# Kernel optimization log

Hardware: AMD Instinct MI355X
Metric: run time of the kernel (lower is better)

## Reference

```python
import jax, jax.numpy as jnp
import numpy as np

EMBED_DIM = 1024
NUM_HEADS = 16
HEAD_DIM = EMBED_DIM // NUM_HEADS


def setup_inputs() -> dict:
    key = jax.random.key(0)
    ks = jax.random.split(key, 11)
    B, T, C = 2, 2048, EMBED_DIM
    s = 1.0 / np.sqrt(C)  # ~ torch Linear init scale
    inp = {
        "q": jax.random.normal(ks[0], (B, T, C), jnp.float32),
        "k": jax.random.normal(ks[1], (B, T, C), jnp.float32),
        "v": jax.random.normal(ks[2], (B, T, C), jnp.float32),
        "Wq": jax.random.normal(ks[3], (C, C), jnp.float32) * s,
        "bq": jax.random.normal(ks[4], (C,), jnp.float32) * s,
        "Wk": jax.random.normal(ks[5], (C, C), jnp.float32) * s,
        "bk": jax.random.normal(ks[6], (C,), jnp.float32) * s,
        "Wv": jax.random.normal(ks[7], (C, C), jnp.float32) * s,
        "bv": jax.random.normal(ks[8], (C,), jnp.float32) * s,
        "Wo": jax.random.normal(ks[9], (C, C), jnp.float32) * s,
        "bo": jax.random.normal(ks[10], (C,), jnp.float32) * s,
    }
    return inp


def _split_heads(x):
    B, T, C = x.shape
    return x.reshape(B, T, NUM_HEADS, HEAD_DIM).transpose(0, 2, 1, 3)  # [B,H,T,Dh]


def reference(q, k, v, Wq, bq, Wk, bk, Wv, bv, Wo, bo):
    B, Tq, C = q.shape
    # torch Linear: y = x @ W.T + b
    qh = _split_heads(q @ Wq.T + bq)
    kh = _split_heads(k @ Wk.T + bk)
    vh = _split_heads(v @ Wv.T + bv)
    scale = 1.0 / np.sqrt(HEAD_DIM).astype(np.float32)
    logits = jnp.einsum("bhqd,bhkd->bhqk", qh, kh) * scale
    attn = jax.nn.softmax(logits, axis=-1)
    out = jnp.einsum("bhqk,bhkd->bhqd", attn, vh)
    out = out.transpose(0, 2, 1, 3).reshape(B, Tq, C)
    return out @ Wo.T + bo
```

## Files before the change

kernel.cpp:

```cpp
#include <hip/hip_runtime.h>
#include <stdint.h>

#define T_SEQ 2048
#define CDIM 1024
#define NHEAD 16
#define HDIM 64
#define MROWS 4096

typedef unsigned short u16;
typedef __attribute__((ext_vector_type(8))) short bf16x8;
typedef __attribute__((ext_vector_type(4))) float f32x4;
typedef __attribute__((ext_vector_type(16))) float f32x16;
typedef __attribute__((ext_vector_type(4))) unsigned short u16x4;
typedef __attribute__((ext_vector_type(4))) unsigned int uint4v;

#if __has_builtin(__builtin_amdgcn_exp2f)
#define EXP2(x) __builtin_amdgcn_exp2f(x)
#else
#define EXP2(x) exp2f(x)
#endif

__device__ __forceinline__ u16 f2bf(float f) {
  unsigned u = __builtin_bit_cast(unsigned, f);
  u += 0x7fffu + ((u >> 16) & 1u);
  return (u16)(u >> 16);
}

__device__ __forceinline__ float bf2f(unsigned hw) {
  return __builtin_bit_cast(float, hw << 16);
}

__device__ __forceinline__ unsigned cvt_pk_bf16(float lo, float hi) {
  unsigned r;
  asm("v_cvt_pk_bf16_f32 %0, %1, %2" : "=v"(r) : "v"(lo), "v"(hi));
  return r;
}

__device__ __forceinline__ void pls(unsigned &a, unsigned &b) {
  asm("v_permlane32_swap_b32 %0, %1" : "+v"(a), "+v"(b));
}

__device__ __forceinline__ void gll16(const void* g, void* l) {
  __builtin_amdgcn_global_load_lds((__attribute__((address_space(1))) void*)(g),
                                   (__attribute__((address_space(3))) void*)(l),
                                   16, 0, 0);
}

__device__ __forceinline__ void wg_barrier() {
  asm volatile("" ::: "memory");
  __builtin_amdgcn_s_barrier();
  asm volatile("" ::: "memory");
}

#define WAIT_VM(N) do { __builtin_amdgcn_s_waitcnt(0xF00 | 0x70 | (N)); \
                        asm volatile("" ::: "memory"); } while (0)

__global__ __launch_bounds__(256)
void cvt_all(const float* __restrict__ q, const float* __restrict__ k, const float* __restrict__ v,
             const float* __restrict__ wq, const float* __restrict__ wk,
             const float* __restrict__ wv, const float* __restrict__ wo,
             u16* __restrict__ qb, u16* __restrict__ kb, u16* __restrict__ vb,
             u16* __restrict__ wqb, u16* __restrict__ wkb, u16* __restrict__ wvb, u16* __restrict__ wob) {
  int b = blockIdx.x;
  const float* src; u16* dst; int base;
  if (b < 1536) {
    int s = b >> 9;
    src = (s == 0) ? q : (s == 1) ? k : v;
    dst = (s == 0) ? qb : (s == 1) ? kb : vb;
    base = (b & 511) * 2048;
  } else {
    int s = (b - 1536) >> 7;
    src = (s == 0) ? wq : (s == 1) ? wk : (s == 2) ? wv : wo;
    dst = (s == 0) ? wqb : (s == 1) ? wkb : (s == 2) ? wvb : wob;
    base = ((b - 1536) & 127) * 2048;
  }
#pragma unroll
  for (int j = 0; j < 8; ++j) {
    int i = base + j * 256 + threadIdx.x;
    float4 a = ((const float4*)src)[i];
    u16x4 o = { f2bf(a.x), f2bf(a.y), f2bf(a.z), f2bf(a.w) };
    ((u16x4*)dst)[i] = o;
  }
}


__device__ __forceinline__ void gemm_stage(const u16* Ag, const u16* Bg, u16* Ad, u16* Bd) {
#pragma unroll
  for (int c = 0; c < 4; ++c) {
    gll16(Ag + c * 32 * CDIM, Ad + c * 2048);
    gll16(Bg + c * 32 * CDIM, Bd + c * 2048);
  }
}

__device__ __forceinline__ void gemm_compute(const u16* As, const u16* Bs,
                                             f32x4 (&acc)[4][4],
                                             int wr, int wc, int lg, int lr) {
#pragma unroll
  for (int kk = 0; kk < 2; ++kk) {
    bf16x8 af[4], bfr[4];
#pragma unroll
    for (int f = 0; f < 4; ++f) {
      int ra = wr * 64 + f * 16 + lr;
      af[f]  = *(const bf16x8*)((const char*)As + ra * 128 + ((lg * 16 + kk * 64) ^ ((ra & 7) << 4)));
      int rb = wc * 64 + f * 16 + lr;
      bfr[f] = *(const bf16x8*)((const char*)Bs + rb * 128 + ((lg * 16 + kk * 64) ^ ((rb & 7) << 4)));
    }
#pragma unroll
    for (int i = 0; i < 4; ++i)
#pragma unroll
      for (int j = 0; j < 4; ++j)
        acc[i][j] = __builtin_amdgcn_mfma_f32_16x16x32_bf16(af[i], bfr[j], acc[i][j], 0, 0, 0);
  }
}

#define GEMM_KLOOP(As, Bs, Ad0, Bd0, Ad1, Bd1)                                 \
  gemm_stage(Ag, Bg, Ad0, Bd0);                                                \
  _Pragma("unroll 1")                                                          \
  for (int kt = 0; kt < 16; ++kt) {                                            \
    wg_barrier();                                                              \
    int nt = (kt + 1 < 16) ? kt + 1 : 15;                                      \
    if (kt & 1) gemm_stage(Ag + nt * 64, Bg + nt * 64, Ad0, Bd0);              \
    else        gemm_stage(Ag + nt * 64, Bg + nt * 64, Ad1, Bd1);              \
    WAIT_VM(8);                                                                \
    wg_barrier();                                                              \
    gemm_compute((kt & 1) ? As[1] : As[0], (kt & 1) ? Bs[1] : Bs[0],           \
                 acc, wr, wc, lg, lr);                                         \
  }

__global__ __launch_bounds__(256)
void gemm_qkv(const u16* __restrict__ A0, const u16* __restrict__ A1, const u16* __restrict__ A2,
              const u16* __restrict__ W0, const u16* __restrict__ W1, const u16* __restrict__ W2,
              const float* __restrict__ b0, const float* __restrict__ b1, const float* __restrict__ b2,
              u16* __restrict__ o0, u16* __restrict__ o1, u16* __restrict__ o2,
              float qscale) {
  __shared__ u16 As[2][128 * 64];
  __shared__ u16 Bs[2][128 * 64];
  const int z = blockIdx.z;
  const u16* A   = (z == 0) ? A0 : (z == 1) ? A1 : A2;
  const u16* Bw  = (z == 0) ? W0 : (z == 1) ? W1 : W2;
  const float* bias = (z == 0) ? b0 : (z == 1) ? b1 : b2;
  u16* outp = (z == 0) ? o0 : (z == 1) ? o1 : o2;
  const float scale = (z == 0) ? qscale : 1.0f;

  const int m0 = blockIdx.y * 128;
  const int n0 = blockIdx.x * 128;
  const int tid = threadIdx.x;
  const int w = tid >> 6, l = tid & 63;
  const int wr = w >> 1, wc = w & 1;
  const int lg = l >> 4, lr = l & 15;

  const int row0 = tid >> 3, slot0 = tid & 7;
  const int so = (slot0 ^ (row0 & 7)) << 3;
  const u16* Ag = A  + ((size_t)(m0 + row0)) * CDIM + so;
  const u16* Bg = Bw + ((size_t)(n0 + row0)) * CDIM + so;
  u16* Ad0 = As[0] + w * 512;  u16* Bd0 = Bs[0] + w * 512;
  u16* Ad1 = As[1] + w * 512;  u16* Bd1 = Bs[1] + w * 512;

  f32x4 acc[4][4] = {};

  GEMM_KLOOP(As, Bs, Ad0, Bd0, Ad1, Bd1)

#pragma unroll
  for (int fj = 0; fj < 4; ++fj) {
    int col = n0 + wc * 64 + fj * 16 + lr;
    float bv = bias[col];
    int h = col >> 6, d = col & 63;
#pragma unroll
    for (int fi = 0; fi < 4; ++fi) {
#pragma unroll
      for (int i = 0; i < 4; ++i) {
        int row = m0 + wr * 64 + fi * 16 + lg * 4 + i;
        float val = (acc[fi][fj][i] + bv) * scale;
        int b = row >> 11, t = row & 2047;
        if (z < 2)
          outp[(((size_t)(b * NHEAD + h)) * T_SEQ + t) * HDIM + d] = f2bf(val);
        else
          outp[(((size_t)(b * NHEAD + h)) * HDIM + d) * T_SEQ + t] = f2bf(val);
      }
    }
  }
}

__global__ __launch_bounds__(256)
void gemm_bt0(const u16* __restrict__ A, const u16* __restrict__ Bw,
              const float* __restrict__ bias, float* __restrict__ outp) {
  __shared__ u16 As[2][128 * 64];
  __shared__ u16 Bs[2][128 * 64];
  const int m0 = blockIdx.y * 128;
  const int n0 = blockIdx.x * 128;
  const int tid = threadIdx.x;
  const int w = tid >> 6, l = tid & 63;
  const int wr = w >> 1, wc = w & 1;
  const int lg = l >> 4, lr = l & 15;

  const int row0 = tid >> 3, slot0 = tid & 7;
  const int so = (slot0 ^ (row0 & 7)) << 3;
  const u16* Ag = A  + ((size_t)(m0 + row0)) * CDIM + so;
  const u16* Bg = Bw + ((size_t)(n0 + row0)) * CDIM + so;
  u16* Ad0 = As[0] + w * 512;  u16* Bd0 = Bs[0] + w * 512;
  u16* Ad1 = As[1] + w * 512;  u16* Bd1 = Bs[1] + w * 512;

  f32x4 acc[4][4] = {};

  GEMM_KLOOP(As, Bs, Ad0, Bd0, Ad1, Bd1)

#pragma unroll
  for (int fj = 0; fj < 4; ++fj) {
    int col = n0 + wc * 64 + fj * 16 + lr;
    float bv = bias[col];
#pragma unroll
    for (int fi = 0; fi < 4; ++fi) {
#pragma unroll
      for (int i = 0; i < 4; ++i) {
        int row = m0 + wr * 64 + fi * 16 + lg * 4 + i;
        outp[(size_t)row * CDIM + col] = acc[fi][fj][i] + bv;
      }
    }
  }
}


__device__ __forceinline__ void attn_tile(const char* Kb, const char* Vb,
                                          const bf16x8 (&qf)[4],
                                          f32x16 (&acc)[2], f32x4& lsum, float& m_run,
                                          int lo5, int hi, int swz) {
  f32x16 s[2] = {};
  const int colK = 16 * hi;
  __builtin_amdgcn_s_setprio(1);
#pragma unroll
  for (int st = 0; st < 4; ++st) {
    bf16x8 k0 = *(const bf16x8*)(Kb + lo5 * 128        + ((32 * st + colK) ^ swz));
    bf16x8 k1 = *(const bf16x8*)(Kb + (lo5 + 32) * 128 + ((32 * st + colK) ^ swz));
    s[0] = __builtin_amdgcn_mfma_f32_32x32x16_bf16(k0, qf[st], s[0], 0, 0, 0);
    s[1] = __builtin_amdgcn_mfma_f32_32x32x16_bf16(k1, qf[st], s[1], 0, 0, 0);
  }
  __builtin_amdgcn_s_setprio(0);

  float t[8];
#pragma unroll
  for (int i = 0; i < 8; ++i)
    t[i] = fmaxf(fmaxf(s[0][2 * i], s[0][2 * i + 1]), fmaxf(s[1][2 * i], s[1][2 * i + 1]));
  float u0 = fmaxf(fmaxf(t[0], t[1]), fmaxf(t[2], t[3]));
  float u1 = fmaxf(fmaxf(t[4], t[5]), fmaxf(t[6], t[7]));
  float tl = fmaxf(u0, u1);
  if (!__all(tl <= m_run + 8.f)) {
    float tmax = fmaxf(tl, __shfl_xor(tl, 32));
    float m_new = fmaxf(m_run, tmax);
    float alpha = EXP2(m_run - m_new);
    lsum[0] *= alpha; lsum[1] *= alpha; lsum[2] *= alpha; lsum[3] *= alpha;
#pragma unroll
    for (int i = 0; i < 16; ++i) { acc[0][i] *= alpha; acc[1][i] *= alpha; }
    m_run = m_new;
  }

  unsigned pg[2][8];
#pragma unroll
  for (int g = 0; g < 8; ++g) {
    float a0 = EXP2(s[0][2 * g] - m_run), b0 = EXP2(s[0][2 * g + 1] - m_run);
    float a1 = EXP2(s[1][2 * g] - m_run), b1 = EXP2(s[1][2 * g + 1] - m_run);
    lsum[g & 3] += (a0 + b0) + (a1 + b1);
    pg[0][g] = cvt_pk_bf16(a0, b0);
    pg[1][g] = cvt_pk_bf16(a1, b1);
  }

  bf16x8 pb[4];
#pragma unroll
  for (int sub = 0; sub < 2; ++sub)
#pragma unroll
    for (int ks = 0; ks < 2; ++ks) {
      unsigned w0 = pg[sub][4 * ks + 0], w1 = pg[sub][4 * ks + 1];
      unsigned w2 = pg[sub][4 * ks + 2], w3 = pg[sub][4 * ks + 3];
      pls(w0, w2); pls(w1, w3);
      uint4v tt = { w0, w1, w2, w3 };
      pb[2 * sub + ks] = __builtin_bit_cast(bf16x8, tt);
    }

  __builtin_amdgcn_s_setprio(1);
#pragma unroll
  for (int ks = 0; ks < 4; ++ks) {
    bf16x8 v0 = *(const bf16x8*)(Vb + lo5 * 128        + ((32 * ks + colK) ^ swz));
    bf16x8 v1 = *(const bf16x8*)(Vb + (lo5 + 32) * 128 + ((32 * ks + colK) ^ swz));
    acc[0] = __builtin_amdgcn_mfma_f32_32x32x16_bf16(v0, pb[ks], acc[0], 0, 0, 0);
    acc[1] = __builtin_amdgcn_mfma_f32_32x32x16_bf16(v1, pb[ks], acc[1], 0, 0, 0);
  }
  __builtin_amdgcn_s_setprio(0);
}

__global__ __launch_bounds__(256, 4)
void attn_fused(const u16* __restrict__ Qh, const u16* __restrict__ Kh,
                const u16* __restrict__ Vt, u16* __restrict__ Op,
                float2* __restrict__ ml) {
  __shared__ u16 Ks[2][64 * 64];
  __shared__ u16 Vs[2][64 * 64];
  const int bh = blockIdx.y;
  const int q0 = blockIdx.x * 128;
  const int half = blockIdx.z;
  const int tid = threadIdx.x;
  const int w = tid >> 6, l = tid & 63;
  const int lo5 = l & 31, hi = l >> 5;
  const int swz = (l & 7) << 4;

  const u16* qptr = Qh + ((size_t)bh * T_SEQ + q0 + w * 32 + lo5) * HDIM + hi * 8;
  bf16x8 qf[4];
#pragma unroll
  for (int s = 0; s < 4; ++s) qf[s] = *(const bf16x8*)(qptr + 16 * s);

  const int srow = (w & 1) * 32 + (l >> 3);
  const int soff = ((l & 7) ^ ((l >> 3) & 7)) << 3;
  const u16* Kgs = Kh + ((size_t)bh * T_SEQ + srow) * HDIM + soff;
  const u16* Vgs = Vt + ((size_t)bh * HDIM + srow) * T_SEQ + soff;
  const int isV = w >> 1;

  auto stage = [&](int t, int db) {
    if (!isV) {
      u16* dst = Ks[db] + (w & 1) * 32 * 64;
      const u16* src = Kgs + (size_t)t * 64 * HDIM;
#pragma unroll
      for (int j = 0; j < 4; ++j)
        gll16(src + j * 8 * HDIM, dst + j * 8 * 64);
    } else {
      u16* dst = Vs[db] + (w & 1) * 32 * 64;
      const u16* src = Vgs + t * 64;
#pragma unroll
      for (int j = 0; j < 4; ++j)
        gll16(src + (size_t)j * 8 * T_SEQ, dst + j * 8 * 64);
    }
  };

  f32x16 acc[2] = {};
  f32x4 lsum = {};
  float m_run = -1e30f;
  const int tb = half * 16;

  stage(tb, 0);
#pragma unroll 1
  for (int s = 0; s < 16; ++s) {
    wg_barrier();
    int ns = (s + 1 < 16) ? s + 1 : 15;
    stage(tb + ns, (s + 1) & 1);
    WAIT_VM(4);
    wg_barrier();
    attn_tile((const char*)Ks[s & 1], (const char*)Vs[s & 1],
              qf, acc, lsum, m_run, lo5, hi, swz);
  }

  float ls = (lsum[0] + lsum[1]) + (lsum[2] + lsum[3]);
  ls += __shfl_xor(ls, 32);
  float inv = 1.f / ls;

  wg_barrier();
  char* os = (char*)&Ks[0][0] + w * 4096;
#pragma unroll
  for (int dsub = 0; dsub < 2; ++dsub)
#pragma unroll
    for (int gg = 0; gg < 4; ++gg) {
      unsigned wa = cvt_pk_bf16(acc[dsub][4 * gg + 0] * inv, acc[dsub][4 * gg + 1] * inv);
      unsigned wb = cvt_pk_bf16(acc[dsub][4 * gg + 2] * inv, acc[dsub][4 * gg + 3] * inv);
      uint2 wv = { wa, wb };
      int byte = lo5 * 128 + (((32 * dsub + 8 * gg + 4 * hi) * 2) ^ swz);
      *(uint2*)(os + byte) = wv;
    }
  u16* orow = Op + ((size_t)(half * 32 + bh) * T_SEQ + q0 + w * 32) * HDIM;
#pragma unroll
  for (int c = 0; c < 4; ++c) {
    int qq = 8 * c + (l >> 3);
    uint4v ov = *(const uint4v*)(os + qq * 128 + ((16 * (l & 7)) ^ ((qq & 7) << 4)));
    *(uint4v*)(orow + qq * HDIM + (l & 7) * 8) = ov;
  }
  if (hi == 0)
    ml[(size_t)(half * 32 + bh) * T_SEQ + q0 + w * 32 + lo5] = make_float2(m_run, ls);
}

__global__ __launch_bounds__(256)
void attn_combine(const u16* __restrict__ Op, const float2* __restrict__ ml,
                  u16* __restrict__ Ao) {
  int task0 = blockIdx.x * 256 + threadIdx.x;
#pragma unroll 1
  for (int it = 0; it < 4; ++it) {
    int task = task0 + it * 131072;
    int chunk = task & 7;
    int q  = (task >> 3) & 2047;
    int bh = task >> 14;
    float2 ml0 = ml[(size_t)bh * T_SEQ + q];
    float2 ml1 = ml[(size_t)(32 + bh) * T_SEQ + q];
    float M = fmaxf(ml0.x, ml1.x);
    float w0 = EXP2(ml0.x - M) * ml0.y;
    float w1 = EXP2(ml1.x - M) * ml1.y;
    float zi = 1.f / (w0 + w1);
    float a0 = w0 * zi, a1 = w1 * zi;
    const u16* p0 = Op + ((size_t)bh * T_SEQ + q) * HDIM + chunk * 8;
    const u16* p1 = Op + ((size_t)(32 + bh) * T_SEQ + q) * HDIM + chunk * 8;
    uint4v o0 = *(const uint4v*)p0;
    uint4v o1 = *(const uint4v*)p1;
    uint4v ov;
#pragma unroll
    for (int j = 0; j < 4; ++j) {
      float lo = a0 * bf2f(o0[j] & 0xffffu)  + a1 * bf2f(o1[j] & 0xffffu);
      float hi = a0 * bf2f(o0[j] >> 16)      + a1 * bf2f(o1[j] >> 16);
      ov[j] = cvt_pk_bf16(lo, hi);
    }
    int b = bh >> 4, h = bh & 15;
    *(uint4v*)(Ao + ((size_t)(b * T_SEQ + q)) * CDIM + h * HDIM + chunk * 8) = ov;
  }
}

extern "C" void kernel_launch(void* const* d_in, const int* in_sizes, int n_in,
                              void* d_out, int out_size, void* d_ws, size_t ws_size,
                              hipStream_t stream) {
  const float* q  = (const float*)d_in[0];
  const float* k  = (const float*)d_in[1];
  const float* v  = (const float*)d_in[2];
  const float* Wq = (const float*)d_in[3];
  const float* bq = (const float*)d_in[4];
  const float* Wk = (const float*)d_in[5];
  const float* bk = (const float*)d_in[6];
  const float* Wv = (const float*)d_in[7];
  const float* bv = (const float*)d_in[8];
  const float* Wo = (const float*)d_in[9];
  const float* bo = (const float*)d_in[10];

  char* ws = (char*)d_ws;
  size_t off = 0;
  auto alloc = [&](size_t n) { void* p = ws + off; off += (n + 255) & ~(size_t)255; return p; };
  const size_t NX = (size_t)MROWS * CDIM;
  const size_t NW = (size_t)CDIM * CDIM;
  u16* qb  = (u16*)alloc(NX * 2);
  u16* kb  = (u16*)alloc(NX * 2);
  u16* vb  = (u16*)alloc(NX * 2);
  u16* Wqb = (u16*)alloc(NW * 2);
  u16* Wkb = (u16*)alloc(NW * 2);
  u16* Wvb = (u16*)alloc(NW * 2);
  u16* Wob = (u16*)alloc(NW * 2);
  u16* Qhp = (u16*)alloc(NX * 2);
  u16* Khp = (u16*)alloc(NX * 2);
  u16* Vtp = (u16*)alloc(NX * 2);
  u16* Aop = (u16*)alloc(NX * 2);

  u16* Op = qb;
  float2* mlp = (float2*)vb;

  cvt_all<<<2048, 256, 0, stream>>>(q, k, v, Wq, Wk, Wv, Wo,
                                    qb, kb, vb, Wqb, Wkb, Wvb, Wob);

  const float qscale = 0.18033688011112042f;
  gemm_qkv<<<dim3(CDIM / 128, MROWS / 128, 3), 256, 0, stream>>>(
      qb, kb, vb, Wqb, Wkb, Wvb, bq, bk, bv, Qhp, Khp, Vtp, qscale);

  attn_fused<<<dim3(T_SEQ / 128, 32, 2), 256, 0, stream>>>(Qhp, Khp, Vtp, Op, mlp);
  attn_combine<<<512, 256, 0, stream>>>(Op, mlp, Aop);

  gemm_bt0<<<dim3(CDIM / 128, MROWS / 128), 256, 0, stream>>>(Aop, Wob, bo, (float*)d_out);

  (void)in_sizes; (void)n_in; (void)out_size; (void)ws_size;
}
```

Baseline: 132.8 us.

## Stage GEMM tiles through registers with single LDS buffer instead of direct-to-LDS loads

```diff
diff --git a/kernel.cpp b/kernel.cpp
--- a/kernel.cpp
+++ b/kernel.cpp
@@ -53,6 +53,8 @@
 }
 
 #define WAIT_VM(N) do { __builtin_amdgcn_s_waitcnt(0xF00 | 0x70 | (N)); \
+                        asm volatile("" ::: "memory"); } while (0)
+#define WAIT_LGKM0 do { __builtin_amdgcn_s_waitcnt(0xC07F); \
                         asm volatile("" ::: "memory"); } while (0)
 
 __global__ __launch_bounds__(256)
@@ -84,11 +86,22 @@
 }
 
 
-__device__ __forceinline__ void gemm_stage(const u16* Ag, const u16* Bg, u16* Ad, u16* Bd) {
+__device__ __forceinline__ void gemm_loads(const u16* Ag, const u16* Bg,
+                                           uint4v (&ar)[4], uint4v (&br)[4]) {
 #pragma unroll
   for (int c = 0; c < 4; ++c) {
-    gll16(Ag + c * 32 * CDIM, Ad + c * 2048);
-    gll16(Bg + c * 32 * CDIM, Bd + c * 2048);
+    ar[c] = *(const uint4v*)(Ag + c * 32 * CDIM);
+    br[c] = *(const uint4v*)(Bg + c * 32 * CDIM);
+  }
+}
+
+__device__ __forceinline__ void gemm_writes(u16* Ad, u16* Bd,
+                                            const uint4v (&ar)[4], const uint4v (&br)[4],
+                                            int tid) {
+#pragma unroll
+  for (int c = 0; c < 4; ++c) {
+    *(uint4v*)(Ad + (size_t)(c * 256 + tid) * 8) = ar[c];
+    *(uint4v*)(Bd + (size_t)(c * 256 + tid) * 8) = br[c];
   }
 }
 
@@ -113,18 +126,25 @@
   }
 }
 
-#define GEMM_KLOOP(As, Bs, Ad0, Bd0, Ad1, Bd1)                                 \
-  gemm_stage(Ag, Bg, Ad0, Bd0);                                                \
+#define GEMM_KLOOP_RS(Asb, Bsb)                                                \
+  uint4v ar[4], br[4];                                                         \
+  gemm_loads(Ag, Bg, ar, br);                                                  \
+  WAIT_VM(0);                                                                  \
+  gemm_writes(Asb, Bsb, ar, br, tid);                                          \
+  WAIT_LGKM0;                                                                  \
+  wg_barrier();                                                                \
   _Pragma("unroll 1")                                                          \
   for (int kt = 0; kt < 16; ++kt) {                                            \
+    int nt = (kt + 1 < 16) ? kt + 1 : 15;                                      \
+    gemm_loads(Ag + nt * 64, Bg + nt * 64, ar, br);                            \
+    gemm_compute(Asb, Bsb, acc, wr, wc, lg, lr);                               \
+    WAIT_VM(0);                                                                \
     wg_barrier();                                                              \
-    int nt = (kt + 1 < 16) ? kt + 1 : 15;                                      \
-    if (kt & 1) gemm_stage(Ag + nt * 64, Bg + nt * 64, Ad0, Bd0);              \
-    else        gemm_stage(Ag + nt * 64, Bg + nt * 64, Ad1, Bd1);              \
-    WAIT_VM(8);                                                                \
-    wg_barrier();                                                              \
-    gemm_compute((kt & 1) ? As[1] : As[0], (kt & 1) ? Bs[1] : Bs[0],           \
-                 acc, wr, wc, lg, lr);                                         \
+    if (kt < 15) {                                                             \
+      gemm_writes(Asb, Bsb, ar, br, tid);                                      \
+      WAIT_LGKM0;                                                              \
+      wg_barrier();                                                            \
+    }                                                                          \
   }
 
 __global__ __launch_bounds__(256)
@@ -133,8 +153,8 @@
               const float* __restrict__ b0, const float* __restrict__ b1, const float* __restrict__ b2,
               u16* __restrict__ o0, u16* __restrict__ o1, u16* __restrict__ o2,
               float qscale) {
-  __shared__ u16 As[2][128 * 64];
-  __shared__ u16 Bs[2][128 * 64];
+  __shared__ u16 Asb[128 * 64];
+  __shared__ u16 Bsb[128 * 64];
   const int z = blockIdx.z;
   const u16* A   = (z == 0) ? A0 : (z == 1) ? A1 : A2;
   const u16* Bw  = (z == 0) ? W0 : (z == 1) ? W1 : W2;
@@ -153,12 +173,10 @@
   const int so = (slot0 ^ (row0 & 7)) << 3;
   const u16* Ag = A  + ((size_t)(m0 + row0)) * CDIM + so;
   const u16* Bg = Bw + ((size_t)(n0 + row0)) * CDIM + so;
-  u16* Ad0 = As[0] + w * 512;  u16* Bd0 = Bs[0] + w * 512;
-  u16* Ad1 = As[1] + w * 512;  u16* Bd1 = Bs[1] + w * 512;
 
   f32x4 acc[4][4] = {};
 
-  GEMM_KLOOP(As, Bs, Ad0, Bd0, Ad1, Bd1)
+  GEMM_KLOOP_RS(Asb, Bsb)
 
 #pragma unroll
   for (int fj = 0; fj < 4; ++fj) {
@@ -184,8 +202,8 @@
 __global__ __launch_bounds__(256)
 void gemm_bt0(const u16* __restrict__ A, const u16* __restrict__ Bw,
               const float* __restrict__ bias, float* __restrict__ outp) {
-  __shared__ u16 As[2][128 * 64];
-  __shared__ u16 Bs[2][128 * 64];
+  __shared__ u16 Asb[128 * 64];
+  __shared__ u16 Bsb[128 * 64];
   const int m0 = blockIdx.y * 128;
   const int n0 = blockIdx.x * 128;
   const int tid = threadIdx.x;
@@ -197,12 +215,10 @@
   const int so = (slot0 ^ (row0 & 7)) << 3;
   const u16* Ag = A  + ((size_t)(m0 + row0)) * CDIM + so;
   const u16* Bg = Bw + ((size_t)(n0 + row0)) * CDIM + so;
-  u16* Ad0 = As[0] + w * 512;  u16* Bd0 = Bs[0] + w * 512;
-  u16* Ad1 = As[1] + w * 512;  u16* Bd1 = Bs[1] + w * 512;
 
   f32x4 acc[4][4] = {};
 
-  GEMM_KLOOP(As, Bs, Ad0, Bd0, Ad1, Bd1)
+  GEMM_KLOOP_RS(Asb, Bsb)
 
 #pragma unroll
   for (int fj = 0; fj < 4; ++fj) {
```

Result: slower. 140.5 us (+5.8%).
